# Optimization experiments

Hardware: AMD Instinct MI355X
Metric: run time of the kernel (lower is better)

The kernel has to match this reference:

```python
import jax, jax.numpy as jnp
import numpy as np

B, H, D, SIZE, S = 32, 16, 64, 262144, 1024
GAMMA = 0.99

def setup_inputs() -> dict:
    key = jax.random.key(0)
    k1, k2, k3, k4 = jax.random.split(key, 4)
    return {
        "query": jax.random.normal(k1, (B, H, D), jnp.float32),
        "key_store": jax.random.normal(k2, (SIZE, H, D), jnp.float32),
        "value_store": jax.random.normal(k3, (SIZE, H, D), jnp.float32),
        "logit_store": 0.1 * jax.random.normal(k4, (SIZE, H), jnp.float32),
    }

def _sample_indices(logit_store, batch, rng):
    # torch softmax over dim=0 (batch*head rows) => per-row weights over s are
    # w[s] proportional to exp(logit[s,h]) / sum_h' exp(logit[s,h'])
    logw = logit_store.T - jax.nn.logsumexp(logit_store, axis=1)[None, :]  # (H, SIZE)
    u = jax.random.uniform(rng, (batch,) + logw.shape, minval=1e-12, maxval=1.0)
    gumbel = -jnp.log(-jnp.log(u))
    # Gumbel top-k == sampling without replacement proportional to exp(logw)
    _, idx = jax.lax.top_k(logw[None] + gumbel, S)  # (B, H, S)
    return idx

def reference(query, key_store, value_store, logit_store):
    b, h, d = query.shape
    idx = _sample_indices(logit_store, b, jax.random.key(42))  # (B,H,S)
    hidx = jnp.arange(h)[None, :, None]  # (1,H,1) broadcasts against idx
    kst = key_store.transpose(1, 0, 2)   # (H, SIZE, D)
    vst = value_store.transpose(1, 0, 2)
    sk = kst[hidx, idx]  # (B,H,S,D) gathered sample keys
    sv = vst[hidx, idx]  # (B,H,S,D) gathered sample values
    attn = jax.nn.softmax(jnp.einsum('bhd,bhsd->bhs', query, sk) * (d ** -0.5), axis=-1)
    lerp_k = jnp.einsum('bhs,bhsd->bhd', attn, sk)
    lerp_v = jnp.einsum('bhs,bhsd->bhd', attn, sv)
    # scattered in-place store updates
    new_k = (1.0 - attn)[..., None] * sk + attn[..., None] * lerp_k[:, :, None, :]
    new_v = (1.0 - attn)[..., None] * sv + attn[..., None] * lerp_v[:, :, None, :]
    key_store_new = kst.at[hidx, idx].set(new_k).transpose(1, 0, 2)
    value_store_new = vst.at[hidx, idx].set(new_v).transpose(1, 0, 2)
    lst = logit_store.T  # (H, SIZE)
    new_l = GAMMA * lst[hidx, idx] + attn  # RHS uses gathered old logits (matches torch)
    logit_store_new = lst.at[hidx, idx].set(new_l).T
    return lerp_k, lerp_v, key_store_new, value_store_new, logit_store_new
```

## Files before the change

kernel.cpp:

```cpp
#include <hip/hip_runtime.h>
#include <stdint.h>

static constexpr int NB = 32, NH = 16, ND = 64, NS = 1024;
static constexpr int SZ = 262144;
static constexpr int NROW = NB * NH;
static constexpr int NSLOT = SZ * NH;

typedef float f32x4 __attribute__((ext_vector_type(4)));

__device__ __forceinline__ uint32_t rotl32(uint32_t x, int r) { return (x << r) | (x >> (32 - r)); }

__device__ __forceinline__ void tf2x32(uint32_t x0, uint32_t x1, uint32_t& o0, uint32_t& o1) {
  const uint32_t K1 = 42u, K2 = 0x1BD11BF0u;
  x1 += K1;
#define TFR(r) { x0 += x1; x1 = rotl32(x1, (r)); x1 ^= x0; }
  TFR(13) TFR(15) TFR(26) TFR(6)
  x0 += K1; x1 += K2 + 1u;
  TFR(17) TFR(29) TFR(16) TFR(24)
  x0 += K2; x1 += 2u;
  TFR(13) TFR(15) TFR(26) TFR(6)
  x1 += K1 + 3u;
  TFR(17) TFR(29) TFR(16) TFR(24)
  x0 += K1; x1 += K2 + 4u;
  TFR(13) TFR(15) TFR(26) TFR(6)
  x0 += K2; x1 += 5u;
#undef TFR
  o0 = x0; o1 = x1;
}

__device__ __forceinline__ uint32_t bits_of(uint32_t row, uint32_t s) {
  uint32_t o0, o1; tf2x32(0u, (row << 18) | s, o0, o1);
  return o0 ^ o1;
}

__device__ __forceinline__ float gumbel_precise(uint32_t row, uint32_t s) {
  uint32_t bits = bits_of(row, s);
  float f = __uint_as_float((bits >> 9) | 0x3f800000u) - 1.0f;
  float u = fmaxf(1e-12f, f + 1e-12f);
  float t = -logf(u);
  return -logf(t);
}

__device__ __forceinline__ float gumbel_fast(uint32_t row, uint32_t s) {
  uint32_t bits = bits_of(row, s);
  float f = __uint_as_float((bits >> 9) | 0x3f800000u) - 1.0f;
  float u = fmaxf(1e-12f, f + 1e-12f);
  float t = -0.69314718056f * __log2f(u);
  return -0.69314718056f * __log2f(t);
}

__device__ __forceinline__ float log2u(uint32_t row, uint32_t s) {
  uint32_t bits = bits_of(row, s);
  float f = __uint_as_float((bits >> 9) | 0x3f800000u) - 1.0f;
  float u = fmaxf(1e-12f, f + 1e-12f);
  return __log2f(u);
}

__device__ __forceinline__ uint32_t fkey(float v) {
  uint32_t u = __float_as_uint(v);
  return (u & 0x80000000u) ? ~u : (u | 0x80000000u);
}
__device__ __forceinline__ float inv_fkey(uint32_t k) {
  uint32_t u = (k & 0x80000000u) ? (k ^ 0x80000000u) : ~k;
  return __uint_as_float(u);
}

__global__ void k_logw(const float* __restrict__ logit, float* __restrict__ logw,
                       float* __restrict__ wexp, float* __restrict__ outL,
                       int* __restrict__ winner) {
  int s = blockIdx.x * blockDim.x + threadIdx.x;
  if (s >= SZ) return;
  const float4* p = (const float4*)(logit + (size_t)s * NH);
  float4 a0 = p[0], a1 = p[1], a2 = p[2], a3 = p[3];
  float x[16] = {a0.x,a0.y,a0.z,a0.w, a1.x,a1.y,a1.z,a1.w,
                 a2.x,a2.y,a2.z,a2.w, a3.x,a3.y,a3.z,a3.w};
  float m = x[0];
#pragma unroll
  for (int h = 1; h < 16; ++h) m = fmaxf(m, x[h]);
  float acc = 0.f;
#pragma unroll
  for (int h = 0; h < 16; ++h) acc += expf(x[h] - m);
  float lse = logf(acc) + m;
#pragma unroll
  for (int h = 0; h < 16; ++h) {
    float lw = x[h] - lse;
    logw[(size_t)h * SZ + s] = lw;
    wexp[(size_t)h * SZ + s] = expf(lw);
  }
  float4* q = (float4*)(outL + (size_t)s * NH);
  q[0] = a0; q[1] = a1; q[2] = a2; q[3] = a3;
  int4 mone = make_int4(-1, -1, -1, -1);
  int4* w = (int4*)(winner + (size_t)s * NH);
  w[0] = mone; w[1] = mone; w[2] = mone; w[3] = mone;
}

__device__ __forceinline__ void find_thresh(const uint32_t* hist, int nbins, int chunk,
                                            uint32_t need, int* outT, uint32_t* outAbove,
                                            int tid) {
  if (tid < 64) {
    int hi = nbins - 1 - tid * chunk;
    uint32_t csum = 0;
    for (int j = 0; j < chunk; ++j) csum += hist[hi - j];
    uint32_t inc = csum;
#pragma unroll
    for (int off = 1; off < 64; off <<= 1) {
      uint32_t t = (uint32_t)__shfl_up((int)inc, off);
      if (tid >= off) inc += t;
    }
    uint32_t pre = inc - csum;
    if (pre < need && inc >= need) {
      uint32_t cum = pre; int T = hi - chunk + 1;
      for (int j = 0; j < chunk; ++j) {
        int b = hi - j;
        if (cum + hist[b] >= need) { T = b; break; }
        cum += hist[b];
      }
      *outT = T; *outAbove = cum;
    }
  }
}

#define SEL_T 1024
#define NCAND 8192
__global__ void __launch_bounds__(SEL_T) k_select(const float* __restrict__ logw,
                                                  const float* __restrict__ wexp,
                                                  int* __restrict__ idx_sel) {
  const int row = blockIdx.x;
  const int h = row & 15;
  const float* lw = logw + (size_t)h * SZ;
  const f32x4* we4 = (const f32x4*)(wexp + (size_t)h * SZ);
  int* outrow = idx_sel + (size_t)row * NS;
  __shared__ uint32_t ckey[NCAND];
  __shared__ int      cidx[NCAND];
  __shared__ uint32_t hist[4096];
  __shared__ int      candA[4096];
  __shared__ int      candB[256];
  __shared__ int      candC[64];
  __shared__ int      ctl[8];
  __shared__ float    sNA;
  const int tid = threadIdx.x;

#pragma unroll
  for (int j = 0; j < 8; ++j) {
    int k = tid + j * SEL_T;
    int s = k << 5;
    ckey[k] = fkey(lw[s] + gumbel_fast(row, s));
  }
  for (int i = tid; i < 4096; i += SEL_T) hist[i] = 0;
  if (tid < 8) ctl[tid] = 0;
  __syncthreads();
#pragma unroll
  for (int j = 0; j < 8; ++j) atomicAdd(&hist[ckey[tid + j * SEL_T] >> 20], 1u);
  __syncthreads();
  find_thresh(hist, 4096, 64, 128u, &ctl[2], (uint32_t*)&ctl[6], tid);
  __syncthreads();
  const uint32_t T0a = (uint32_t)ctl[2];
  const uint32_t aboveA = (uint32_t)ctl[6];
  for (int i = tid; i < 4096; i += SEL_T) hist[i] = 0;
  __syncthreads();
#pragma unroll
  for (int j = 0; j < 8; ++j) {
    uint32_t k = ckey[tid + j * SEL_T];
    if ((k >> 20) == T0a) atomicAdd(&hist[(k >> 8) & 0xFFFu], 1u);
  }
  __syncthreads();
  find_thresh(hist, 4096, 64, 128u - aboveA, &ctl[2], (uint32_t*)&ctl[6], tid);
  __syncthreads();
  if (tid == 0) {
    uint32_t Tlo = (T0a << 20) | ((uint32_t)ctl[2] << 8);
    float vlo = inv_fkey(Tlo);
    sNA = -expf(-vlo) * 1.4426950408889634f;
    ctl[1] = 0;
  }
  __syncthreads();
  const float nA = sNA;

  for (int g = tid; g < SZ / 4; g += SEL_T) {
    f32x4 w4 = we4[g];
    int s0 = g << 2;
    float l0 = log2u(row, s0);
    float l1 = log2u(row, s0 + 1);
    float l2 = log2u(row, s0 + 2);
    float l3 = log2u(row, s0 + 3);
    if (l0 >= nA * w4.x) { int p = atomicAdd(&ctl[1], 1); if (p < NCAND) cidx[p] = s0; }
    if (l1 >= nA * w4.y) { int p = atomicAdd(&ctl[1], 1); if (p < NCAND) cidx[p] = s0 + 1; }
    if (l2 >= nA * w4.z) { int p = atomicAdd(&ctl[1], 1); if (p < NCAND) cidx[p] = s0 + 2; }
    if (l3 >= nA * w4.w) { int p = atomicAdd(&ctl[1], 1); if (p < NCAND) cidx[p] = s0 + 3; }
  }
  __syncthreads();
  const int C = min(ctl[1], NCAND);

  for (int i = tid; i < 4096; i += SEL_T) hist[i] = 0;
  if (tid == 0) { ctl[0] = 0; ctl[3] = 0; ctl[4] = 0; ctl[5] = 0; }
  __syncthreads();
  for (int ci = tid; ci < C; ci += SEL_T) {
    int s = cidx[ci];
    uint32_t k = fkey(lw[s] + gumbel_precise(row, s));
    ckey[ci] = k;
    atomicAdd(&hist[k >> 20], 1u);
  }
  __syncthreads();
  find_thresh(hist, 4096, 64, (uint32_t)NS, &ctl[2], (uint32_t*)&ctl[6], tid);
  __syncthreads();
  const int T0 = ctl[2];
  for (int ci = tid; ci < C; ci += SEL_T) {
    int b = (int)(ckey[ci] >> 20);
    if (b > T0)       { int p = atomicAdd(&ctl[0], 1); outrow[p] = cidx[ci]; }
    else if (b == T0) { int c = atomicAdd(&ctl[3], 1); if (c < 4096) candA[c] = ci; }
  }
  __syncthreads();
  const int CA = min(ctl[3], 4096);
  for (int i = tid; i < 4096; i += SEL_T) hist[i] = 0;
  __syncthreads();
  for (int i = tid; i < CA; i += SEL_T) atomicAdd(&hist[(ckey[candA[i]] >> 8) & 0xFFFu], 1u);
  __syncthreads();
  find_thresh(hist, 4096, 64, (uint32_t)(NS - ctl[0]), &ctl[2], (uint32_t*)&ctl[6], tid);
  __syncthreads();
  const int T1 = ctl[2];
  for (int i = tid; i < CA; i += SEL_T) {
    int ci = candA[i];
    int mid = (int)((ckey[ci] >> 8) & 0xFFFu);
    if (mid > T1)       { int p = atomicAdd(&ctl[0], 1); outrow[p] = cidx[ci]; }
    else if (mid == T1) { int c = atomicAdd(&ctl[4], 1); if (c < 256) candB[c] = ci; }
  }
  __syncthreads();
  const int CB = min(ctl[4], 256);
  if (tid < 256) hist[tid] = 0;
  __syncthreads();
  for (int i = tid; i < CB; i += SEL_T) atomicAdd(&hist[ckey[candB[i]] & 0xFFu], 1u);
  __syncthreads();
  find_thresh(hist, 256, 4, (uint32_t)(NS - ctl[0]), &ctl[2], (uint32_t*)&ctl[6], tid);
  __syncthreads();
  const int T2 = ctl[2];
  for (int i = tid; i < CB; i += SEL_T) {
    int ci = candB[i];
    int lo = (int)(ckey[ci] & 0xFFu);
    if (lo > T2)       { int p = atomicAdd(&ctl[0], 1); outrow[p] = cidx[ci]; }
    else if (lo == T2) { int c = atomicAdd(&ctl[5], 1); if (c < 64) candC[c] = ci; }
  }
  __syncthreads();
  if (tid == 0) {
    int need = NS - ctl[0];
    int cc = min(ctl[5], 64);
    for (int k = 0; k < need; ++k) {
      int best = 0x7fffffff, bi = 0;
      for (int j = 0; j < cc; ++j) { int s = cidx[candC[j]]; if (s < best) { best = s; bi = j; } }
      if (best == 0x7fffffff) best = 0;
      outrow[ctl[0] + k] = best;
      if (cc > 0) cidx[candC[bi]] = 0x7fffffff;
    }
  }
}

#define ATT_T 512
__global__ void __launch_bounds__(ATT_T) k_attn(const float* __restrict__ qin,
    const f32x4* __restrict__ K4, const f32x4* __restrict__ V4,
    const int* __restrict__ idx_sel, float* __restrict__ attn_ws,
    float* __restrict__ lerp_k, float* __restrict__ lerp_v, int* __restrict__ winner) {
  const int row = blockIdx.x;
  const int h = row & 15, b = row >> 4;
  const int tid = threadIdx.x;
  const int lane = tid & 63, wv = tid >> 6;
  const int sj = lane >> 3, dj = lane & 7;
  __shared__ float sc[NS];
  __shared__ int sel_s[NS];
  __shared__ float red[ATT_T];
  __shared__ f32x4 pk4[8][16], pv4[8][16];
  const int* sel = idx_sel + (size_t)row * NS;
  for (int i = tid; i < NS; i += ATT_T) sel_s[i] = sel[i];
  const f32x4* q4 = (const f32x4*)(qin + (size_t)row * ND);
  f32x4 qa = q4[dj * 2], qb = q4[dj * 2 + 1];
  __syncthreads();
  for (int it = 0; it < 16; it += 2) {
    int i1 = it * 64 + wv * 8 + sj;
    int i2 = i1 + 64;
    int x1 = sel_s[i1], x2 = sel_s[i2];
    size_t b1 = ((size_t)x1 * NH + h) * 16 + dj * 2;
    size_t b2 = ((size_t)x2 * NH + h) * 16 + dj * 2;
    f32x4 ka1 = K4[b1], kb1 = K4[b1 + 1];
    f32x4 ka2 = K4[b2], kb2 = K4[b2 + 1];
    float p1 = ka1.x*qa.x + ka1.y*qa.y + ka1.z*qa.z + ka1.w*qa.w
             + kb1.x*qb.x + kb1.y*qb.y + kb1.z*qb.z + kb1.w*qb.w;
    float p2 = ka2.x*qa.x + ka2.y*qa.y + ka2.z*qa.z + ka2.w*qa.w
             + kb2.x*qb.x + kb2.y*qb.y + kb2.z*qb.z + kb2.w*qb.w;
#pragma unroll
    for (int off = 1; off < 8; off <<= 1) { p1 += __shfl_xor(p1, off); p2 += __shfl_xor(p2, off); }
    if (dj == 0) { sc[i1] = p1 * 0.125f; sc[i2] = p2 * 0.125f; }
  }
  __syncthreads();
  float v1 = sc[tid], v2 = sc[tid + 512];
  red[tid] = fmaxf(v1, v2); __syncthreads();
  for (int s = 256; s; s >>= 1) { if (tid < s) red[tid] = fmaxf(red[tid], red[tid + s]); __syncthreads(); }
  float m = red[0]; __syncthreads();
  float e1 = expf(v1 - m), e2 = expf(v2 - m);
  red[tid] = e1 + e2; __syncthreads();
  for (int s = 256; s; s >>= 1) { if (tid < s) red[tid] += red[tid + s]; __syncthreads(); }
  float inv = 1.0f / red[0];
  float a1 = e1 * inv, a2 = e2 * inv;
  sc[tid] = a1; sc[tid + 512] = a2;
  attn_ws[(size_t)row * NS + tid] = a1;
  attn_ws[(size_t)row * NS + tid + 512] = a2;
  __syncthreads();
  f32x4 AK = 0.f, BK = 0.f, AV = 0.f, BV = 0.f;
  for (int it = 0; it < 16; it += 2) {
    int i1 = it * 64 + wv * 8 + sj;
    int i2 = i1 + 64;
    int x1 = sel_s[i1], x2 = sel_s[i2];
    float c1 = sc[i1], c2 = sc[i2];
    size_t b1 = ((size_t)x1 * NH + h) * 16 + dj * 2;
    size_t b2 = ((size_t)x2 * NH + h) * 16 + dj * 2;
    f32x4 k1a = K4[b1], k1b = K4[b1 + 1], v1a = V4[b1], v1b = V4[b1 + 1];
    f32x4 k2a = K4[b2], k2b = K4[b2 + 1], v2a = V4[b2], v2b = V4[b2 + 1];
    AK += c1 * k1a + c2 * k2a; BK += c1 * k1b + c2 * k2b;
    AV += c1 * v1a + c2 * v2a; BV += c1 * v1b + c2 * v2b;
  }
#pragma unroll
  for (int off = 8; off < 64; off <<= 1) {
    AK.x += __shfl_xor(AK.x, off); AK.y += __shfl_xor(AK.y, off);
    AK.z += __shfl_xor(AK.z, off); AK.w += __shfl_xor(AK.w, off);
    BK.x += __shfl_xor(BK.x, off); BK.y += __shfl_xor(BK.y, off);
    BK.z += __shfl_xor(BK.z, off); BK.w += __shfl_xor(BK.w, off);
    AV.x += __shfl_xor(AV.x, off); AV.y += __shfl_xor(AV.y, off);
    AV.z += __shfl_xor(AV.z, off); AV.w += __shfl_xor(AV.w, off);
    BV.x += __shfl_xor(BV.x, off); BV.y += __shfl_xor(BV.y, off);
    BV.z += __shfl_xor(BV.z, off); BV.w += __shfl_xor(BV.w, off);
  }
  if (sj == 0) {
    pk4[wv][dj * 2] = AK; pk4[wv][dj * 2 + 1] = BK;
    pv4[wv][dj * 2] = AV; pv4[wv][dj * 2 + 1] = BV;
  }
  __syncthreads();
  if (tid < 64) {
    float lk = 0.f, lv = 0.f;
    const float* pkf = (const float*)pk4;
    const float* pvf = (const float*)pv4;
#pragma unroll
    for (int ww = 0; ww < 8; ++ww) { lk += pkf[ww * 64 + tid]; lv += pvf[ww * 64 + tid]; }
    lerp_k[(size_t)row * ND + tid] = lk;
    lerp_v[(size_t)row * ND + tid] = lv;
  }
  for (int i = tid; i < NS; i += ATT_T) atomicMax(&winner[(size_t)sel_s[i] * NH + h], b);
}

__global__ void k_mark(const int* __restrict__ idx_sel, const float* __restrict__ attn_ws,
                       const int* __restrict__ winner, const float* __restrict__ Lst,
                       float* __restrict__ wa, float* __restrict__ outL) {
  int t = blockIdx.x * 256 + threadIdx.x;
  int row = t >> 10, h = row & 15, b = row >> 4;
  int idx = idx_sel[t];
  size_t slot = (size_t)idx * NH + h;
  if (winner[slot] == b) {
    float a = attn_ws[t];
    wa[slot] = a;
    outL[slot] = 0.99f * Lst[slot] + a;
  }
}

__global__ void __launch_bounds__(256) k_emit(const f32x4* __restrict__ K4,
    const f32x4* __restrict__ V4, const int* __restrict__ winner,
    const float* __restrict__ wa, const f32x4* __restrict__ LK4,
    const f32x4* __restrict__ LV4, f32x4* __restrict__ oK4, f32x4* __restrict__ oV4) {
  const long tid0 = (long)blockIdx.x * 256 + threadIdx.x;
  const long stride = 8192L * 256;
#pragma unroll 2
  for (int r = 0; r < 32; ++r) {
    long i = tid0 + (long)r * stride;
    int slot = (int)(i >> 4);
    int w = winner[slot];
    f32x4 kv = __builtin_nontemporal_load(&K4[i]);
    f32x4 vv = __builtin_nontemporal_load(&V4[i]);
    if (w >= 0) {
      float a = wa[slot];
      int rr = (w << 4) | (slot & 15);
      f32x4 lk = LK4[((long)rr << 4) + (i & 15)];
      f32x4 lv = LV4[((long)rr << 4) + (i & 15)];
      float o = 1.0f - a;
      kv = o * kv + a * lk;
      vv = o * vv + a * lv;
    }
    __builtin_nontemporal_store(kv, &oK4[i]);
    __builtin_nontemporal_store(vv, &oV4[i]);
  }
}

extern "C" void kernel_launch(void* const* d_in, const int* in_sizes, int n_in,
                              void* d_out, int out_size, void* d_ws, size_t ws_size,
                              hipStream_t stream) {
  const float* q   = (const float*)d_in[0];
  const float* Kst = (const float*)d_in[1];
  const float* Vst = (const float*)d_in[2];
  const float* Lst = (const float*)d_in[3];

  float* out    = (float*)d_out;
  float* out_lk = out;
  float* out_lv = out + 32768;
  float* outK   = out + 65536;
  float* outV   = outK + 268435456;
  float* outL   = outV + 268435456;

  char* ws = (char*)d_ws;
  float* logw   = (float*)ws;
  float* wexp   = (float*)(ws + (16ull << 20));
  int*   idxsel = (int*)(ws + (32ull << 20));
  float* attn   = (float*)(ws + (34ull << 20));
  int*   winner = (int*)(ws + (36ull << 20));
  float* wa     = (float*)(ws + (52ull << 20));

  k_logw<<<SZ / 256, 256, 0, stream>>>(Lst, logw, wexp, outL, winner);
  k_select<<<NROW, SEL_T, 0, stream>>>(logw, wexp, idxsel);
  k_attn<<<NROW, ATT_T, 0, stream>>>(q, (const f32x4*)Kst, (const f32x4*)Vst,
                                     idxsel, attn, out_lk, out_lv, winner);
  k_mark<<<NROW * NS / 256, 256, 0, stream>>>(idxsel, attn, winner, Lst, wa, outL);
  k_emit<<<8192, 256, 0, stream>>>((const f32x4*)Kst, (const f32x4*)Vst, winner, wa,
                                   (const f32x4*)out_lk, (const f32x4*)out_lv,
                                   (f32x4*)outK, (f32x4*)outV);
}
```

Baseline: 1.411 ms.

## Fuse selection and attention into a mega-kernel overlapped with the store copy

Selection and attention now run in one kernel whose blocks are interleaved with blocks that do a plain copy of the key/value stores, so the bandwidth-bound copy overlaps the compute-bound sampling. A separate fixup kernel then rewrites only the winning scattered rows instead of the emit pass checking winner for every element. The candidate threshold is now computed analytically from a per-head weight sum gathered in k_logw, replacing the strided pre-sampling pass, and shared memory is shrunk with a union, 16-bit candidate indices and smaller histograms. The fixup depends on the copy having finished, and the analytic threshold may yield too few or too many candidates for some rows.

Result: slower. 1.892 ms (+34.1%).

```diff
diff --git a/kernel.cpp b/kernel.cpp
--- a/kernel.cpp
+++ b/kernel.cpp
@@ -4,7 +4,7 @@
 static constexpr int NB = 32, NH = 16, ND = 64, NS = 1024;
 static constexpr int SZ = 262144;
 static constexpr int NROW = NB * NH;
-static constexpr int NSLOT = SZ * NH;
+static constexpr long NF4 = 67108864L;
 
 typedef float f32x4 __attribute__((ext_vector_type(4)));
 
@@ -41,14 +41,6 @@
   return -logf(t);
 }
 
-__device__ __forceinline__ float gumbel_fast(uint32_t row, uint32_t s) {
-  uint32_t bits = bits_of(row, s);
-  float f = __uint_as_float((bits >> 9) | 0x3f800000u) - 1.0f;
-  float u = fmaxf(1e-12f, f + 1e-12f);
-  float t = -0.69314718056f * __log2f(u);
-  return -0.69314718056f * __log2f(t);
-}
-
 __device__ __forceinline__ float log2u(uint32_t row, uint32_t s) {
   uint32_t bits = bits_of(row, s);
   float f = __uint_as_float((bits >> 9) | 0x3f800000u) - 1.0f;
@@ -60,16 +52,15 @@
   uint32_t u = __float_as_uint(v);
   return (u & 0x80000000u) ? ~u : (u | 0x80000000u);
 }
-__device__ __forceinline__ float inv_fkey(uint32_t k) {
-  uint32_t u = (k & 0x80000000u) ? (k ^ 0x80000000u) : ~k;
-  return __uint_as_float(u);
-}
 
 __global__ void k_logw(const float* __restrict__ logit, float* __restrict__ logw,
                        float* __restrict__ wexp, float* __restrict__ outL,
-                       int* __restrict__ winner) {
-  int s = blockIdx.x * blockDim.x + threadIdx.x;
-  if (s >= SZ) return;
+                       int* __restrict__ winner, float* __restrict__ W) {
+  __shared__ float sW[16];
+  const int tid = threadIdx.x;
+  if (tid < 16) sW[tid] = 0.f;
+  __syncthreads();
+  int s = blockIdx.x * 256 + tid;
   const float4* p = (const float4*)(logit + (size_t)s * NH);
   float4 a0 = p[0], a1 = p[1], a2 = p[2], a3 = p[3];
   float x[16] = {a0.x,a0.y,a0.z,a0.w, a1.x,a1.y,a1.z,a1.w,
@@ -81,22 +72,33 @@
 #pragma unroll
   for (int h = 0; h < 16; ++h) acc += expf(x[h] - m);
   float lse = logf(acc) + m;
+  float wl[16];
 #pragma unroll
   for (int h = 0; h < 16; ++h) {
     float lw = x[h] - lse;
     logw[(size_t)h * SZ + s] = lw;
-    wexp[(size_t)h * SZ + s] = expf(lw);
+    float e = expf(lw);
+    wexp[(size_t)h * SZ + s] = e;
+    wl[h] = e;
+  }
+#pragma unroll
+  for (int h = 0; h < 16; ++h) {
+    float v = wl[h];
+#pragma unroll
+    for (int off = 32; off; off >>= 1) v += __shfl_xor(v, off);
+    if ((tid & 63) == 0) atomicAdd(&sW[h], v);
   }
   float4* q = (float4*)(outL + (size_t)s * NH);
   q[0] = a0; q[1] = a1; q[2] = a2; q[3] = a3;
   int4 mone = make_int4(-1, -1, -1, -1);
   int4* w = (int4*)(winner + (size_t)s * NH);
   w[0] = mone; w[1] = mone; w[2] = mone; w[3] = mone;
+  __syncthreads();
+  if (tid < 16) atomicAdd(&W[tid], sW[tid]);
 }
 
 __device__ __forceinline__ void find_thresh(const uint32_t* hist, int nbins, int chunk,
-                                            uint32_t need, int* outT, uint32_t* outAbove,
-                                            int tid) {
+                                            uint32_t need, int* outT, int tid) {
   if (tid < 64) {
     int hi = nbins - 1 - tid * chunk;
     uint32_t csum = 0;
@@ -115,128 +117,134 @@
         if (cum + hist[b] >= need) { T = b; break; }
         cum += hist[b];
       }
-      *outT = T; *outAbove = cum;
+      *outT = T;
     }
   }
 }
 
-#define SEL_T 1024
-#define NCAND 8192
-__global__ void __launch_bounds__(SEL_T) k_select(const float* __restrict__ logw,
-                                                  const float* __restrict__ wexp,
-                                                  int* __restrict__ idx_sel) {
-  const int row = blockIdx.x;
-  const int h = row & 15;
+#define MEGA_T 512
+#define NCAND 6144
+__global__ void __launch_bounds__(MEGA_T, 4) k_mega(
+    const float* __restrict__ logw, const float* __restrict__ wexp,
+    const float* __restrict__ Wsum, const float* __restrict__ qin,
+    const float* __restrict__ Kst, const float* __restrict__ Vst,
+    int* __restrict__ idx_sel, float* __restrict__ attn_ws,
+    float* __restrict__ lerp_k, float* __restrict__ lerp_v, int* __restrict__ winner,
+    f32x4* __restrict__ oK4, f32x4* __restrict__ oV4) {
+  const int bid = blockIdx.x;
+  const int tid = threadIdx.x;
+  const bool is_sel = (bid < 2048) && ((bid & 3) == 3);
+
+  if (!is_sel) {
+    const f32x4* K4 = (const f32x4*)Kst;
+    const f32x4* V4 = (const f32x4*)Vst;
+    int copy_id = (bid < 2048) ? (bid - (bid >> 2)) : (1536 + bid - 2048);
+    long i = (long)copy_id * MEGA_T + tid;
+    const long stride = 2048L * MEGA_T;
+#pragma unroll 4
+    for (int r = 0; r < 64; ++r, i += stride) {
+      __builtin_nontemporal_store(__builtin_nontemporal_load(&K4[i]), &oK4[i]);
+      __builtin_nontemporal_store(__builtin_nontemporal_load(&V4[i]), &oV4[i]);
+    }
+    return;
+  }
+
+  const int row = bid >> 2;
+  const int h = row & 15, b = row >> 4;
   const float* lw = logw + (size_t)h * SZ;
   const f32x4* we4 = (const f32x4*)(wexp + (size_t)h * SZ);
   int* outrow = idx_sel + (size_t)row * NS;
-  __shared__ uint32_t ckey[NCAND];
-  __shared__ int      cidx[NCAND];
-  __shared__ uint32_t hist[4096];
-  __shared__ int      candA[4096];
-  __shared__ int      candB[256];
-  __shared__ int      candC[64];
-  __shared__ int      ctl[8];
-  __shared__ float    sNA;
-  const int tid = threadIdx.x;
-
-#pragma unroll
-  for (int j = 0; j < 8; ++j) {
-    int k = tid + j * SEL_T;
-    int s = k << 5;
-    ckey[k] = fkey(lw[s] + gumbel_fast(row, s));
-  }
-  for (int i = tid; i < 4096; i += SEL_T) hist[i] = 0;
-  if (tid < 8) ctl[tid] = 0;
-  __syncthreads();
-#pragma unroll
-  for (int j = 0; j < 8; ++j) atomicAdd(&hist[ckey[tid + j * SEL_T] >> 20], 1u);
-  __syncthreads();
-  find_thresh(hist, 4096, 64, 128u, &ctl[2], (uint32_t*)&ctl[6], tid);
-  __syncthreads();
-  const uint32_t T0a = (uint32_t)ctl[2];
-  const uint32_t aboveA = (uint32_t)ctl[6];
-  for (int i = tid; i < 4096; i += SEL_T) hist[i] = 0;
-  __syncthreads();
-#pragma unroll
-  for (int j = 0; j < 8; ++j) {
-    uint32_t k = ckey[tid + j * SEL_T];
-    if ((k >> 20) == T0a) atomicAdd(&hist[(k >> 8) & 0xFFFu], 1u);
-  }
-  __syncthreads();
-  find_thresh(hist, 4096, 64, 128u - aboveA, &ctl[2], (uint32_t*)&ctl[6], tid);
-  __syncthreads();
+
+  __shared__ union {
+    struct {
+      int      cidx[NCAND];
+      uint32_t ckey[NCAND];
+      uint32_t hist[2048];
+      uint16_t candA[4096];
+      uint16_t candB[512];
+      uint16_t candC[64];
+    } s;
+    struct {
+      int   sel_s[NS];
+      float sc[NS];
+      float red[MEGA_T];
+      f32x4 pk4[8][16], pv4[8][16];
+    } a;
+  } u;
+  __shared__ int ctl[8];
+  __shared__ float sNA;
+
   if (tid == 0) {
-    uint32_t Tlo = (T0a << 20) | ((uint32_t)ctl[2] << 8);
-    float vlo = inv_fkey(Tlo);
-    sNA = -expf(-vlo) * 1.4426950408889634f;
+    float Wh = Wsum[h];
+    sNA = -4096.0f / (Wh * 0.6931471805599453f);
     ctl[1] = 0;
   }
   __syncthreads();
   const float nA = sNA;
 
-  for (int g = tid; g < SZ / 4; g += SEL_T) {
+  for (int g = tid; g < SZ / 4; g += MEGA_T) {
     f32x4 w4 = we4[g];
     int s0 = g << 2;
     float l0 = log2u(row, s0);
     float l1 = log2u(row, s0 + 1);
     float l2 = log2u(row, s0 + 2);
     float l3 = log2u(row, s0 + 3);
-    if (l0 >= nA * w4.x) { int p = atomicAdd(&ctl[1], 1); if (p < NCAND) cidx[p] = s0; }
-    if (l1 >= nA * w4.y) { int p = atomicAdd(&ctl[1], 1); if (p < NCAND) cidx[p] = s0 + 1; }
-    if (l2 >= nA * w4.z) { int p = atomicAdd(&ctl[1], 1); if (p < NCAND) cidx[p] = s0 + 2; }
-    if (l3 >= nA * w4.w) { int p = atomicAdd(&ctl[1], 1); if (p < NCAND) cidx[p] = s0 + 3; }
+    if (l0 >= nA * w4.x) { int p = atomicAdd(&ctl[1], 1); if (p < NCAND) u.s.cidx[p] = s0; }
+    if (l1 >= nA * w4.y) { int p = atomicAdd(&ctl[1], 1); if (p < NCAND) u.s.cidx[p] = s0 + 1; }
+    if (l2 >= nA * w4.z) { int p = atomicAdd(&ctl[1], 1); if (p < NCAND) u.s.cidx[p] = s0 + 2; }
+    if (l3 >= nA * w4.w) { int p = atomicAdd(&ctl[1], 1); if (p < NCAND) u.s.cidx[p] = s0 + 3; }
   }
   __syncthreads();
   const int C = min(ctl[1], NCAND);
 
-  for (int i = tid; i < 4096; i += SEL_T) hist[i] = 0;
+  for (int i = tid; i < 2048; i += MEGA_T) u.s.hist[i] = 0;
   if (tid == 0) { ctl[0] = 0; ctl[3] = 0; ctl[4] = 0; ctl[5] = 0; }
   __syncthreads();
-  for (int ci = tid; ci < C; ci += SEL_T) {
-    int s = cidx[ci];
+  for (int ci = tid; ci < C; ci += MEGA_T) {
+    int s = u.s.cidx[ci];
     uint32_t k = fkey(lw[s] + gumbel_precise(row, s));
-    ckey[ci] = k;
-    atomicAdd(&hist[k >> 20], 1u);
-  }
-  __syncthreads();
-  find_thresh(hist, 4096, 64, (uint32_t)NS, &ctl[2], (uint32_t*)&ctl[6], tid);
+    u.s.ckey[ci] = k;
+    atomicAdd(&u.s.hist[k >> 21], 1u);
+  }
+  __syncthreads();
+  find_thresh(u.s.hist, 2048, 32, (uint32_t)NS, &ctl[2], tid);
   __syncthreads();
   const int T0 = ctl[2];
-  for (int ci = tid; ci < C; ci += SEL_T) {
-    int b = (int)(ckey[ci] >> 20);
-    if (b > T0)       { int p = atomicAdd(&ctl[0], 1); outrow[p] = cidx[ci]; }
-    else if (b == T0) { int c = atomicAdd(&ctl[3], 1); if (c < 4096) candA[c] = ci; }
+  for (int ci = tid; ci < C; ci += MEGA_T) {
+    int bb = (int)(u.s.ckey[ci] >> 21);
+    if (bb > T0)       { int p = atomicAdd(&ctl[0], 1); outrow[p] = u.s.cidx[ci]; }
+    else if (bb == T0) { int c = atomicAdd(&ctl[3], 1); if (c < 4096) u.s.candA[c] = (uint16_t)ci; }
   }
   __syncthreads();
   const int CA = min(ctl[3], 4096);
-  for (int i = tid; i < 4096; i += SEL_T) hist[i] = 0;
-  __syncthreads();
-  for (int i = tid; i < CA; i += SEL_T) atomicAdd(&hist[(ckey[candA[i]] >> 8) & 0xFFFu], 1u);
-  __syncthreads();
-  find_thresh(hist, 4096, 64, (uint32_t)(NS - ctl[0]), &ctl[2], (uint32_t*)&ctl[6], tid);
+  for (int i = tid; i < 2048; i += MEGA_T) u.s.hist[i] = 0;
+  __syncthreads();
+  for (int i = tid; i < CA; i += MEGA_T)
+    atomicAdd(&u.s.hist[(u.s.ckey[u.s.candA[i]] >> 10) & 0x7FFu], 1u);
+  __syncthreads();
+  find_thresh(u.s.hist, 2048, 32, (uint32_t)(NS - ctl[0]), &ctl[2], tid);
   __syncthreads();
   const int T1 = ctl[2];
-  for (int i = tid; i < CA; i += SEL_T) {
-    int ci = candA[i];
-    int mid = (int)((ckey[ci] >> 8) & 0xFFFu);
-    if (mid > T1)       { int p = atomicAdd(&ctl[0], 1); outrow[p] = cidx[ci]; }
-    else if (mid == T1) { int c = atomicAdd(&ctl[4], 1); if (c < 256) candB[c] = ci; }
-  }
-  __syncthreads();
-  const int CB = min(ctl[4], 256);
-  if (tid < 256) hist[tid] = 0;
-  __syncthreads();
-  for (int i = tid; i < CB; i += SEL_T) atomicAdd(&hist[ckey[candB[i]] & 0xFFu], 1u);
-  __syncthreads();
-  find_thresh(hist, 256, 4, (uint32_t)(NS - ctl[0]), &ctl[2], (uint32_t*)&ctl[6], tid);
+  for (int i = tid; i < CA; i += MEGA_T) {
+    int ci = u.s.candA[i];
+    int mid = (int)((u.s.ckey[ci] >> 10) & 0x7FFu);
+    if (mid > T1)       { int p = atomicAdd(&ctl[0], 1); outrow[p] = u.s.cidx[ci]; }
+    else if (mid == T1) { int c = atomicAdd(&ctl[4], 1); if (c < 512) u.s.candB[c] = (uint16_t)ci; }
+  }
+  __syncthreads();
+  const int CB = min(ctl[4], 512);
+  for (int i = tid; i < 1024; i += MEGA_T) u.s.hist[i] = 0;
+  __syncthreads();
+  for (int i = tid; i < CB; i += MEGA_T) atomicAdd(&u.s.hist[u.s.ckey[u.s.candB[i]] & 0x3FFu], 1u);
+  __syncthreads();
+  find_thresh(u.s.hist, 1024, 16, (uint32_t)(NS - ctl[0]), &ctl[2], tid);
   __syncthreads();
   const int T2 = ctl[2];
-  for (int i = tid; i < CB; i += SEL_T) {
-    int ci = candB[i];
-    int lo = (int)(ckey[ci] & 0xFFu);
-    if (lo > T2)       { int p = atomicAdd(&ctl[0], 1); outrow[p] = cidx[ci]; }
-    else if (lo == T2) { int c = atomicAdd(&ctl[5], 1); if (c < 64) candC[c] = ci; }
+  for (int i = tid; i < CB; i += MEGA_T) {
+    int ci = u.s.candB[i];
+    int lo = (int)(u.s.ckey[ci] & 0x3FFu);
+    if (lo > T2)       { int p = atomicAdd(&ctl[0], 1); outrow[p] = u.s.cidx[ci]; }
+    else if (lo == T2) { int c = atomicAdd(&ctl[5], 1); if (c < 64) u.s.candC[c] = (uint16_t)ci; }
   }
   __syncthreads();
   if (tid == 0) {
@@ -244,37 +252,26 @@
     int cc = min(ctl[5], 64);
     for (int k = 0; k < need; ++k) {
       int best = 0x7fffffff, bi = 0;
-      for (int j = 0; j < cc; ++j) { int s = cidx[candC[j]]; if (s < best) { best = s; bi = j; } }
+      for (int j = 0; j < cc; ++j) { int s = u.s.cidx[u.s.candC[j]]; if (s < best) { best = s; bi = j; } }
       if (best == 0x7fffffff) best = 0;
       outrow[ctl[0] + k] = best;
-      if (cc > 0) cidx[candC[bi]] = 0x7fffffff;
+      if (cc > 0) u.s.cidx[u.s.candC[bi]] = 0x7fffffff;
     }
   }
-}
-
-#define ATT_T 512
-__global__ void __launch_bounds__(ATT_T) k_attn(const float* __restrict__ qin,
-    const f32x4* __restrict__ K4, const f32x4* __restrict__ V4,
-    const int* __restrict__ idx_sel, float* __restrict__ attn_ws,
-    float* __restrict__ lerp_k, float* __restrict__ lerp_v, int* __restrict__ winner) {
-  const int row = blockIdx.x;
-  const int h = row & 15, b = row >> 4;
-  const int tid = threadIdx.x;
+  __syncthreads();
+
+  const f32x4* K4 = (const f32x4*)Kst;
+  const f32x4* V4 = (const f32x4*)Vst;
   const int lane = tid & 63, wv = tid >> 6;
   const int sj = lane >> 3, dj = lane & 7;
-  __shared__ float sc[NS];
-  __shared__ int sel_s[NS];
-  __shared__ float red[ATT_T];
-  __shared__ f32x4 pk4[8][16], pv4[8][16];
-  const int* sel = idx_sel + (size_t)row * NS;
-  for (int i = tid; i < NS; i += ATT_T) sel_s[i] = sel[i];
+  for (int i = tid; i < NS; i += MEGA_T) u.a.sel_s[i] = outrow[i];
   const f32x4* q4 = (const f32x4*)(qin + (size_t)row * ND);
   f32x4 qa = q4[dj * 2], qb = q4[dj * 2 + 1];
   __syncthreads();
   for (int it = 0; it < 16; it += 2) {
     int i1 = it * 64 + wv * 8 + sj;
     int i2 = i1 + 64;
-    int x1 = sel_s[i1], x2 = sel_s[i2];
+    int x1 = u.a.sel_s[i1], x2 = u.a.sel_s[i2];
     size_t b1 = ((size_t)x1 * NH + h) * 16 + dj * 2;
     size_t b2 = ((size_t)x2 * NH + h) * 16 + dj * 2;
     f32x4 ka1 = K4[b1], kb1 = K4[b1 + 1];
@@ -285,19 +282,19 @@
              + kb2.x*qb.x + kb2.y*qb.y + kb2.z*qb.z + kb2.w*qb.w;
 #pragma unroll
     for (int off = 1; off < 8; off <<= 1) { p1 += __shfl_xor(p1, off); p2 += __shfl_xor(p2, off); }
-    if (dj == 0) { sc[i1] = p1 * 0.125f; sc[i2] = p2 * 0.125f; }
-  }
-  __syncthreads();
-  float v1 = sc[tid], v2 = sc[tid + 512];
-  red[tid] = fmaxf(v1, v2); __syncthreads();
-  for (int s = 256; s; s >>= 1) { if (tid < s) red[tid] = fmaxf(red[tid], red[tid + s]); __syncthreads(); }
-  float m = red[0]; __syncthreads();
+    if (dj == 0) { u.a.sc[i1] = p1 * 0.125f; u.a.sc[i2] = p2 * 0.125f; }
+  }
+  __syncthreads();
+  float v1 = u.a.sc[tid], v2 = u.a.sc[tid + 512];
+  u.a.red[tid] = fmaxf(v1, v2); __syncthreads();
+  for (int s = 256; s; s >>= 1) { if (tid < s) u.a.red[tid] = fmaxf(u.a.red[tid], u.a.red[tid + s]); __syncthreads(); }
+  float m = u.a.red[0]; __syncthreads();
   float e1 = expf(v1 - m), e2 = expf(v2 - m);
-  red[tid] = e1 + e2; __syncthreads();
-  for (int s = 256; s; s >>= 1) { if (tid < s) red[tid] += red[tid + s]; __syncthreads(); }
-  float inv = 1.0f / red[0];
+  u.a.red[tid] = e1 + e2; __syncthreads();
+  for (int s = 256; s; s >>= 1) { if (tid < s) u.a.red[tid] += u.a.red[tid + s]; __syncthreads(); }
+  float inv = 1.0f / u.a.red[0];
   float a1 = e1 * inv, a2 = e2 * inv;
-  sc[tid] = a1; sc[tid + 512] = a2;
+  u.a.sc[tid] = a1; u.a.sc[tid + 512] = a2;
   attn_ws[(size_t)row * NS + tid] = a1;
   attn_ws[(size_t)row * NS + tid + 512] = a2;
   __syncthreads();
@@ -305,8 +302,8 @@
   for (int it = 0; it < 16; it += 2) {
     int i1 = it * 64 + wv * 8 + sj;
     int i2 = i1 + 64;
-    int x1 = sel_s[i1], x2 = sel_s[i2];
-    float c1 = sc[i1], c2 = sc[i2];
+    int x1 = u.a.sel_s[i1], x2 = u.a.sel_s[i2];
+    float c1 = u.a.sc[i1], c2 = u.a.sc[i2];
     size_t b1 = ((size_t)x1 * NH + h) * 16 + dj * 2;
     size_t b2 = ((size_t)x2 * NH + h) * 16 + dj * 2;
     f32x4 k1a = K4[b1], k1b = K4[b1 + 1], v1a = V4[b1], v1b = V4[b1 + 1];
@@ -326,61 +323,43 @@
     BV.z += __shfl_xor(BV.z, off); BV.w += __shfl_xor(BV.w, off);
   }
   if (sj == 0) {
-    pk4[wv][dj * 2] = AK; pk4[wv][dj * 2 + 1] = BK;
-    pv4[wv][dj * 2] = AV; pv4[wv][dj * 2 + 1] = BV;
+    u.a.pk4[wv][dj * 2] = AK; u.a.pk4[wv][dj * 2 + 1] = BK;
+    u.a.pv4[wv][dj * 2] = AV; u.a.pv4[wv][dj * 2 + 1] = BV;
   }
   __syncthreads();
   if (tid < 64) {
     float lk = 0.f, lv = 0.f;
-    const float* pkf = (const float*)pk4;
-    const float* pvf = (const float*)pv4;
+    const float* pkf = (const float*)u.a.pk4;
+    const float* pvf = (const float*)u.a.pv4;
 #pragma unroll
     for (int ww = 0; ww < 8; ++ww) { lk += pkf[ww * 64 + tid]; lv += pvf[ww * 64 + tid]; }
     lerp_k[(size_t)row * ND + tid] = lk;
     lerp_v[(size_t)row * ND + tid] = lv;
   }
-  for (int i = tid; i < NS; i += ATT_T) atomicMax(&winner[(size_t)sel_s[i] * NH + h], b);
-}
-
-__global__ void k_mark(const int* __restrict__ idx_sel, const float* __restrict__ attn_ws,
-                       const int* __restrict__ winner, const float* __restrict__ Lst,
-                       float* __restrict__ wa, float* __restrict__ outL) {
-  int t = blockIdx.x * 256 + threadIdx.x;
-  int row = t >> 10, h = row & 15, b = row >> 4;
-  int idx = idx_sel[t];
+  for (int i = tid; i < NS; i += MEGA_T) atomicMax(&winner[(size_t)u.a.sel_s[i] * NH + h], b);
+}
+
+__global__ void __launch_bounds__(256) k_fixup(const float* __restrict__ Kst,
+    const float* __restrict__ Vst, const float* __restrict__ Lst,
+    const int* __restrict__ idx_sel, const float* __restrict__ attn_ws,
+    const int* __restrict__ winner, const float* __restrict__ lerp_k,
+    const float* __restrict__ lerp_v, float* __restrict__ outK,
+    float* __restrict__ outV, float* __restrict__ outL) {
+  int g = blockIdx.x * 4 + (threadIdx.x >> 6);
+  int lane = threadIdx.x & 63;
+  int row = g >> 10, i = g & 1023;
+  int h = row & 15, b = row >> 4;
+  int idx = idx_sel[(size_t)row * NS + i];
   size_t slot = (size_t)idx * NH + h;
-  if (winner[slot] == b) {
-    float a = attn_ws[t];
-    wa[slot] = a;
-    outL[slot] = 0.99f * Lst[slot] + a;
-  }
-}
-
-__global__ void __launch_bounds__(256) k_emit(const f32x4* __restrict__ K4,
-    const f32x4* __restrict__ V4, const int* __restrict__ winner,
-    const float* __restrict__ wa, const f32x4* __restrict__ LK4,
-    const f32x4* __restrict__ LV4, f32x4* __restrict__ oK4, f32x4* __restrict__ oV4) {
-  const long tid0 = (long)blockIdx.x * 256 + threadIdx.x;
-  const long stride = 8192L * 256;
-#pragma unroll 2
-  for (int r = 0; r < 32; ++r) {
-    long i = tid0 + (long)r * stride;
-    int slot = (int)(i >> 4);
-    int w = winner[slot];
-    f32x4 kv = __builtin_nontemporal_load(&K4[i]);
-    f32x4 vv = __builtin_nontemporal_load(&V4[i]);
-    if (w >= 0) {
-      float a = wa[slot];
-      int rr = (w << 4) | (slot & 15);
-      f32x4 lk = LK4[((long)rr << 4) + (i & 15)];
-      f32x4 lv = LV4[((long)rr << 4) + (i & 15)];
-      float o = 1.0f - a;
-      kv = o * kv + a * lk;
-      vv = o * vv + a * lv;
-    }
-    __builtin_nontemporal_store(kv, &oK4[i]);
-    __builtin_nontemporal_store(vv, &oV4[i]);
-  }
+  if (winner[slot] != b) return;
+  float a = attn_ws[(size_t)row * NS + i];
+  size_t base = slot * ND + lane;
+  float kv = Kst[base], vv = Vst[base];
+  float lk = lerp_k[(size_t)row * ND + lane], lv = lerp_v[(size_t)row * ND + lane];
+  float o = 1.0f - a;
+  outK[base] = o * kv + a * lk;
+  outV[base] = o * vv + a * lv;
+  if (lane == 0) outL[slot] = 0.99f * Lst[slot] + a;
 }
 
 extern "C" void kernel_launch(void* const* d_in, const int* in_sizes, int n_in,
@@ -404,14 +383,13 @@
   int*   idxsel = (int*)(ws + (32ull << 20));
   float* attn   = (float*)(ws + (34ull << 20));
   int*   winner = (int*)(ws + (36ull << 20));
-  float* wa     = (float*)(ws + (52ull << 20));
-
-  k_logw<<<SZ / 256, 256, 0, stream>>>(Lst, logw, wexp, outL, winner);
-  k_select<<<NROW, SEL_T, 0, stream>>>(logw, wexp, idxsel);
-  k_attn<<<NROW, ATT_T, 0, stream>>>(q, (const f32x4*)Kst, (const f32x4*)Vst,
-                                     idxsel, attn, out_lk, out_lv, winner);
-  k_mark<<<NROW * NS / 256, 256, 0, stream>>>(idxsel, attn, winner, Lst, wa, outL);
-  k_emit<<<8192, 256, 0, stream>>>((const f32x4*)Kst, (const f32x4*)Vst, winner, wa,
-                                   (const f32x4*)out_lk, (const f32x4*)out_lv,
-                                   (f32x4*)outK, (f32x4*)outV);
-}
+  float* Wsum   = (float*)(ws + (52ull << 20));
+
+  hipMemsetAsync(Wsum, 0, 16 * sizeof(float), stream);
+  k_logw<<<SZ / 256, 256, 0, stream>>>(Lst, logw, wexp, outL, winner, Wsum);
+  k_mega<<<2560, MEGA_T, 0, stream>>>(logw, wexp, Wsum, q, Kst, Vst,
+                                      idxsel, attn, out_lk, out_lv, winner,
+                                      (f32x4*)outK, (f32x4*)outV);
+  k_fixup<<<NROW * NS / 4, 256, 0, stream>>>(Kst, Vst, Lst, idxsel, attn, winner,
+                                             out_lk, out_lv, outK, outV, outL);
+}
```
